# Optimization experiments

Measured on AMD Instinct MI355X. Metric: run time of the kernel, lower is better.

The kernel has to match this reference:

```python
import jax, jax.numpy as jnp
import numpy as np

B, S, H, DK = 2, 2048, 16, 64
D = H * DK  # d_model = 1024


def setup_inputs() -> dict:
    key = jax.random.key(0)
    ks = jax.random.split(key, 12)
    inp = {
        "queries": jax.random.normal(ks[0], (B, S, D), jnp.float32),
        "keys": jax.random.normal(ks[1], (B, S, D), jnp.float32),
        "values": jax.random.normal(ks[2], (B, S, D), jnp.float32),
        # additive 0/1 mask (1 = masked out), causal upper-triangular
        "mask": jnp.triu(jnp.ones((S, S), jnp.float32), k=1)[None, None, :, :],
        "W_q": jax.random.normal(ks[3], (D, D), jnp.float32) / np.sqrt(D),
        "b_q": jnp.zeros((D,), jnp.float32),
        "W_k": jax.random.normal(ks[4], (D, D), jnp.float32) / np.sqrt(D),
        "b_k": jnp.zeros((D,), jnp.float32),
        "W_v": jax.random.normal(ks[5], (D, D), jnp.float32) / np.sqrt(D),
        "b_v": jnp.zeros((D,), jnp.float32),
        "W_o": jax.random.normal(ks[6], (D, D), jnp.float32) / np.sqrt(D),
        "b_o": jnp.zeros((D,), jnp.float32),
    }
    return inp


def _split_heads(x):
    # (B, S, D) -> (B, H, S, DK)
    return x.reshape(x.shape[0], x.shape[1], H, DK).transpose(0, 2, 1, 3)


def reference(queries, keys, values, mask, W_q, b_q, W_k, b_k, W_v, b_v, W_o, b_o):
    q = _split_heads(queries @ W_q + b_q)  # (B, H, S, DK)
    k = _split_heads(keys @ W_k + b_k)
    v = _split_heads(values @ W_v + b_v)
    scale = 1.0 / jnp.sqrt(jnp.asarray(DK, q.dtype))
    scores = jnp.einsum("bhqd,bhkd->bhqk", q, k) * scale  # (B, H, S, S)
    scores = scores + (-1e9) * mask
    weights = jax.nn.softmax(scores, axis=-1)
    o = jnp.einsum("bhqk,bhkd->bhqd", weights, v)  # (B, H, S, DK)
    o = o.transpose(0, 2, 1, 3).reshape(queries.shape[0], queries.shape[1], D)
    return o @ W_o + b_o
```

## Files before the change

### kernel.cpp

```cpp
#include <hip/hip_runtime.h>
#include <hip/hip_bf16.h>
#include <stdint.h>

typedef unsigned short u16;
typedef __attribute__((ext_vector_type(4))) float f32x4;
typedef __attribute__((ext_vector_type(8))) short bf16x8;

#define B_ 2
#define S_ 2048
#define H_ 16
#define D_ 1024
#define XELEMS (B_*S_*D_)
#define WELEMS (D_*D_)
#define QSCALE 0.18033688f

__device__ __forceinline__ u16 f2bf(float f) {
  union { float f; unsigned u; } v; v.f = f;
  unsigned r = v.u + 0x7fffu + ((v.u >> 16) & 1u);
  return (u16)(r >> 16);
}

__device__ __forceinline__ void async16(const void* g, void* l) {
  __builtin_amdgcn_global_load_lds(
      (const __attribute__((address_space(1))) unsigned int*)g,
      (__attribute__((address_space(3))) unsigned int*)l, 16, 0, 0);
}

#if __has_builtin(__builtin_amdgcn_exp2f)
#define EXP2(x) __builtin_amdgcn_exp2f(x)
#else
#define EXP2(x) exp2f(x)
#endif

__device__ __forceinline__ unsigned cvtpk(float a, float b) {
  unsigned r;
  asm("v_cvt_pk_bf16_f32 %0, %1, %2" : "=v"(r) : "v"(a), "v"(b));
  return r;
}

__global__ __launch_bounds__(256) void prep_k(
    const float* __restrict__ q, const float* __restrict__ k,
    const float* __restrict__ v,
    const float* __restrict__ Wq, const float* __restrict__ Wk,
    const float* __restrict__ Wv, const float* __restrict__ Wo,
    u16* __restrict__ X, u16* __restrict__ WT) {
  const int bid = blockIdx.x;
  if (bid < 4096) {
    __shared__ float tile[32][33];
    const int z = bid >> 10, rem = bid & 1023;
    const float* W = (z == 0) ? Wq : (z == 1) ? Wk : (z == 2) ? Wv : Wo;
    u16* o = WT + z * WELEMS;
    const int r0 = (rem >> 5) << 5, c0 = (rem & 31) << 5;
    const int tx = threadIdx.x & 31, ty = threadIdx.x >> 5;
    #pragma unroll
    for (int rr = ty; rr < 32; rr += 8)
      tile[rr][tx] = W[(r0 + rr) * D_ + c0 + tx];
    __syncthreads();
    #pragma unroll
    for (int rr = ty; rr < 32; rr += 8)
      o[(c0 + rr) * D_ + r0 + tx] = f2bf(tile[tx][rr]);
  } else {
    const int cb = bid - 4096;
    const int ngrp = XELEMS / 8;
    const int total = 3 * ngrp;
    for (int i = cb * 256 + threadIdx.x; i < total; i += 1024 * 256) {
      int which = i / ngrp;
      int off = (i - which * ngrp) * 8;
      const float* src = (which == 0) ? q : (which == 1) ? k : v;
      float4 a = *(const float4*)(src + off);
      float4 b = *(const float4*)(src + off + 4);
      u16 rr[8] = {f2bf(a.x), f2bf(a.y), f2bf(a.z), f2bf(a.w),
                   f2bf(b.x), f2bf(b.y), f2bf(b.z), f2bf(b.w)};
      uint4 pk;
      pk.x = (unsigned)rr[0] | ((unsigned)rr[1] << 16);
      pk.y = (unsigned)rr[2] | ((unsigned)rr[3] << 16);
      pk.z = (unsigned)rr[4] | ((unsigned)rr[5] << 16);
      pk.w = (unsigned)rr[6] | ((unsigned)rr[7] << 16);
      *(uint4*)(X + which * XELEMS + off) = pk;
    }
  }
}

template <int MODE, int DBUF>
__device__ __forceinline__ void gemm_body(const u16* __restrict__ A,
                                          const u16* __restrict__ BT,
                                          const float* __restrict__ bias,
                                          void* __restrict__ outp,
                                          int bm, int bn, float scale) {
  constexpr int SMEM_BYTES = DBUF ? 65536 : (MODE == 2 ? 34816 : 32768);
  __shared__ __align__(16) char smem[SMEM_BYTES];
  const int tid = threadIdx.x;
  const int w = tid >> 6, l = tid & 63;
  const int wr = w >> 1, wc = w & 1;
  const int g = l >> 4, r = l & 15;
  (void)w; (void)l;

  f32x4 acc[4][4];
  #pragma unroll
  for (int i = 0; i < 4; i++)
    #pragma unroll
    for (int j = 0; j < 4; j++) acc[i][j] = (f32x4){0.f, 0.f, 0.f, 0.f};

  int dst[4], aoff[4], boff[4];
  #pragma unroll
  for (int i = 0; i < 4; i++) {
    const int o = i * 4096 + tid * 16;
    dst[i] = o;
    const int row = o >> 7;
    const int cbyte = (o & 127) ^ ((row & 7) << 4);
    aoff[i] = (bm + row) * 1024 + (cbyte >> 1);
    boff[i] = (bn + row) * 1024 + (cbyte >> 1);
  }

  if (DBUF == 0) {
    char* Ab = smem;
    char* Bb = smem + 16384;
    for (int t = 0; t < 16; ++t) {
      const int k0 = t * 64;
      #pragma unroll
      for (int i = 0; i < 4; i++) async16(A + aoff[i] + k0, Ab + dst[i]);
      #pragma unroll
      for (int i = 0; i < 4; i++) async16(BT + boff[i] + k0, Bb + dst[i]);
      __syncthreads();
      bf16x8 af[2][4], bf[2][4];
      #pragma unroll
      for (int kk = 0; kk < 2; kk++)
        #pragma unroll
        for (int mi = 0; mi < 4; mi++) {
          const int rA = wr * 64 + mi * 16 + r;
          af[kk][mi] = *(const bf16x8*)(Ab +
              ((rA * 128 + kk * 64 + g * 16) ^ ((rA & 7) << 4)));
        }
      #pragma unroll
      for (int kk = 0; kk < 2; kk++)
        #pragma unroll
        for (int ni = 0; ni < 4; ni++) {
          const int rB = wc * 64 + ni * 16 + r;
          bf[kk][ni] = *(const bf16x8*)(Bb +
              ((rB * 128 + kk * 64 + g * 16) ^ ((rB & 7) << 4)));
        }
      #pragma unroll
      for (int kk = 0; kk < 2; kk++)
        #pragma unroll
        for (int mi = 0; mi < 4; mi++)
          #pragma unroll
          for (int ni = 0; ni < 4; ni++)
            acc[mi][ni] = __builtin_amdgcn_mfma_f32_16x16x32_bf16(
                af[kk][mi], bf[kk][ni], acc[mi][ni], 0, 0, 0);
      __syncthreads();
    }
  } else {
    #pragma unroll
    for (int i = 0; i < 4; i++) {
      async16(A + aoff[i], smem + dst[i]);
      async16(BT + boff[i], smem + 16384 + dst[i]);
    }
    for (int t = 0; t < 16; ++t) {
      const int buf = t & 1;
      const char* Ab = smem + buf * 32768;
      const char* Bb = Ab + 16384;
      if (t < 15) {
        const int k0 = (t + 1) * 64;
        char* An = smem + (buf ^ 1) * 32768;
        #pragma unroll
        for (int i = 0; i < 4; i++) {
          async16(A + aoff[i] + k0, An + dst[i]);
          async16(BT + boff[i] + k0, An + 16384 + dst[i]);
        }
        asm volatile("s_waitcnt vmcnt(8)" ::: "memory");
      } else {
        asm volatile("s_waitcnt vmcnt(0)" ::: "memory");
      }
      asm volatile("s_barrier" ::: "memory");

      bf16x8 af[2][4], bf[2][4];
      #pragma unroll
      for (int kk = 0; kk < 2; kk++)
        #pragma unroll
        for (int mi = 0; mi < 4; mi++) {
          const int rA = wr * 64 + mi * 16 + r;
          af[kk][mi] = *(const bf16x8*)(Ab +
              ((rA * 128 + kk * 64 + g * 16) ^ ((rA & 7) << 4)));
        }
      #pragma unroll
      for (int kk = 0; kk < 2; kk++)
        #pragma unroll
        for (int ni = 0; ni < 4; ni++) {
          const int rB = wc * 64 + ni * 16 + r;
          bf[kk][ni] = *(const bf16x8*)(Bb +
              ((rB * 128 + kk * 64 + g * 16) ^ ((rB & 7) << 4)));
        }
      __builtin_amdgcn_s_setprio(1);
      #pragma unroll
      for (int kk = 0; kk < 2; kk++)
        #pragma unroll
        for (int mi = 0; mi < 4; mi++)
          #pragma unroll
          for (int ni = 0; ni < 4; ni++)
            acc[mi][ni] = __builtin_amdgcn_mfma_f32_16x16x32_bf16(
                af[kk][mi], bf[kk][ni], acc[mi][ni], 0, 0, 0);
      __builtin_amdgcn_s_setprio(0);
      asm volatile("s_barrier" ::: "memory");
    }
  }

  const int col0 = bn + wc * 64;
  float bc[4];
  #pragma unroll
  for (int ni = 0; ni < 4; ni++) bc[ni] = bias[col0 + ni * 16 + r];

  if (MODE == 0) {
    u16* out = (u16*)outp;
    #pragma unroll
    for (int mi = 0; mi < 4; mi++) {
      const int row = bm + wr * 64 + mi * 16 + g * 4;
      #pragma unroll
      for (int ni = 0; ni < 4; ni++) {
        const int col = col0 + ni * 16 + r;
        const int h = col >> 6, dk = col & 63;
        #pragma unroll
        for (int i = 0; i < 4; i++) {
          const int rr = row + i;
          const int b = rr >> 11, s = rr & 2047;
          out[(((b << 4) | h) * 2048 + s) * 64 + dk] =
              f2bf((acc[mi][ni][i] + bc[ni]) * scale);
        }
      }
    }
  } else if (MODE == 2) {
    u16* Ts = (u16*)smem;
    #pragma unroll
    for (int mi = 0; mi < 4; mi++) {
      const int lrow = wr * 64 + mi * 16 + g * 4;
      #pragma unroll
      for (int ni = 0; ni < 4; ni++) {
        const int lcol = wc * 64 + ni * 16 + r;
        u16 p0 = f2bf(acc[mi][ni][0] + bc[ni]);
        u16 p1 = f2bf(acc[mi][ni][1] + bc[ni]);
        u16 p2 = f2bf(acc[mi][ni][2] + bc[ni]);
        u16 p3 = f2bf(acc[mi][ni][3] + bc[ni]);
        uint2 pk;
        pk.x = (unsigned)p0 | ((unsigned)p1 << 16);
        pk.y = (unsigned)p2 | ((unsigned)p3 << 16);
        *(uint2*)&Ts[lcol * 136 + lrow] = pk;
      }
    }
    __syncthreads();
    u16* out = (u16*)outp;
    const int bb = bm >> 11;
    const int sbase = bm & 2047;
    #pragma unroll
    for (int j = 0; j < 8; j++) {
      const int c = (tid >> 6) * 512 + j * 64 + (tid & 63);
      const int dk = c >> 4, sc = c & 15;
      const int col = bn + dk;
      const int h = col >> 6, dkk = col & 63;
      bf16x8 vv = *(const bf16x8*)&Ts[dk * 136 + sc * 8];
      *(bf16x8*)&out[(((size_t)(((bb << 4) | h) * 64 + dkk)) << 11) +
                     sbase + sc * 8] = vv;
    }
  } else {
    float* out = (float*)outp;
    #pragma unroll
    for (int mi = 0; mi < 4; mi++) {
      const int row = bm + wr * 64 + mi * 16 + g * 4;
      #pragma unroll
      for (int ni = 0; ni < 4; ni++) {
        const int col = col0 + ni * 16 + r;
        #pragma unroll
        for (int i = 0; i < 4; i++)
          out[(row + i) * 1024 + col] = acc[mi][ni][i] + bc[ni];
      }
    }
  }
}

__global__ __launch_bounds__(256) void gemm_qkv_k(
    const u16* __restrict__ X, const u16* __restrict__ WT,
    const float* __restrict__ bq, const float* __restrict__ bk,
    const float* __restrict__ bv, u16* __restrict__ QKV) {
  const int z = blockIdx.z;
  const float* bias = (z == 0) ? bq : (z == 1) ? bk : bv;
  if (z == 2)
    gemm_body<2, 0>(X + z * XELEMS, WT + z * WELEMS, bias, QKV + z * XELEMS,
                    blockIdx.x * 128, blockIdx.y * 128, 1.0f);
  else
    gemm_body<0, 0>(X + z * XELEMS, WT + z * WELEMS, bias, QKV + z * XELEMS,
                    blockIdx.x * 128, blockIdx.y * 128,
                    (z == 0) ? QSCALE : 1.0f);
}

__global__ __launch_bounds__(256) void gemm_o_k(
    const u16* __restrict__ O, const u16* __restrict__ WOT,
    const float* __restrict__ bo, float* __restrict__ out) {
  gemm_body<1, 1>(O, WOT, bo, out, blockIdx.x * 128, blockIdx.y * 128, 1.0f);
}

__global__ __launch_bounds__(512) void attn_k(
    const u16* __restrict__ Qh, const u16* __restrict__ Kh,
    const u16* __restrict__ VTh, u16* __restrict__ O) {
  __shared__ __align__(16) char ldsK[2][8192];
  __shared__ __align__(16) char ldsV[2][8192];
  __shared__ __align__(16) u16 ldsP[8][16 * 72];

  const int bh = blockIdx.y;
  const int pj = blockIdx.x;
  const int tid = threadIdx.x;
  const int w = tid >> 6, l = tid & 63;
  const int grp = w >> 2, wg = w & 3;
  const int g = l >> 4, r = l & 15;
  const int b = bh >> 4, h = bh & 15;

  const u16* Qp = Qh + bh * (S_ * 64);
  const char* Kp = (const char*)(Kh + bh * (S_ * 64));
  const char* Vp = (const char*)(VTh + bh * (64 * S_));

  const int o = w * 1024 + l * 16;
  const int kdst = o;
  const int ksrc = o ^ (((o >> 7) & 7) << 4);
  const int vd = o >> 7, vcb = o & 127;
  const int vfix = vd * (S_ * 2) + (vcb ^ ((vd & 7) << 4));
  u16* Pq = &ldsP[w][0];

  const int qt = grp ? (31 - pj) : pj;
  const int q0w = qt * 64 + wg * 16;
  const int my_nt = qt + 1;
  const int nt_max = 32 - pj;
  const int qloc = wg * 16 + r;

  bf16x8 qf[2];
  #pragma unroll
  for (int dh = 0; dh < 2; dh++)
    qf[dh] = *(const bf16x8*)(Qp + (q0w + r) * 64 + dh * 32 + g * 8);
  asm volatile("s_waitcnt vmcnt(0)" ::: "memory");

  f32x4 accT[4];
  #pragma unroll
  for (int dn = 0; dn < 4; dn++) accT[dn] = (f32x4){0.f, 0.f, 0.f, 0.f};
  float mrun = -1e30f, lsum = 0.f;

  async16(Kp + ksrc, &ldsK[0][0] + kdst);
  async16(Vp + vfix, &ldsV[0][0] + kdst);

  for (int t = 0; t < nt_max; ++t) {
    const int buf = t & 1;
    if (t + 1 < nt_max) {
      async16(Kp + (t + 1) * 8192 + ksrc, &ldsK[buf ^ 1][0] + kdst);
      async16(Vp + (t + 1) * 128 + vfix, &ldsV[buf ^ 1][0] + kdst);
      asm volatile("s_waitcnt vmcnt(2)" ::: "memory");
    } else {
      asm volatile("s_waitcnt vmcnt(0)" ::: "memory");
    }
    asm volatile("s_barrier" ::: "memory");

    if (t < my_nt) {
      const char* Kb = &ldsK[buf][0];
      f32x4 sc[4];
      #pragma unroll
      for (int ct = 0; ct < 4; ct++) {
        const int row = ct * 16 + r;
        const int sw = (row & 7) << 4;
        bf16x8 k0 = *(const bf16x8*)(Kb + ((row * 128 + g * 16) ^ sw));
        bf16x8 k1 = *(const bf16x8*)(Kb + ((row * 128 + 64 + g * 16) ^ sw));
        f32x4 z = (f32x4){0.f, 0.f, 0.f, 0.f};
        z = __builtin_amdgcn_mfma_f32_16x16x32_bf16(k0, qf[0], z, 0, 0, 0);
        sc[ct] = __builtin_amdgcn_mfma_f32_16x16x32_bf16(k1, qf[1], z, 0, 0, 0);
      }

      if (t == my_nt - 1) {
        #pragma unroll
        for (int ct = 0; ct < 4; ct++)
          #pragma unroll
          for (int i = 0; i < 4; i++)
            if (ct * 16 + g * 4 + i > qloc) sc[ct][i] = -1e9f;
      }

      float a0 = fmaxf(fmaxf(sc[0][0], sc[0][1]), sc[0][2]);
      float a1 = fmaxf(fmaxf(sc[0][3], sc[1][0]), sc[1][1]);
      float a2 = fmaxf(fmaxf(sc[1][2], sc[1][3]), sc[2][0]);
      float a3 = fmaxf(fmaxf(sc[2][1], sc[2][2]), sc[2][3]);
      float a4 = fmaxf(fmaxf(sc[3][0], sc[3][1]), sc[3][2]);
      float pmax = fmaxf(fmaxf(fmaxf(a0, a1), fmaxf(a2, a3)),
                         fmaxf(a4, sc[3][3]));
      pmax = fmaxf(pmax, __shfl_xor(pmax, 16, 64));
      pmax = fmaxf(pmax, __shfl_xor(pmax, 32, 64));

      if (!__all(pmax - mrun <= 11.0f)) {
        const float mnew = fmaxf(mrun, pmax);
        const float corr = EXP2(mrun - mnew);
        mrun = mnew;
        #pragma unroll
        for (int dn = 0; dn < 4; dn++)
          #pragma unroll
          for (int i = 0; i < 4; i++) accT[dn][i] *= corr;
        lsum *= corr;
      }

      float ps = 0.f;
      #pragma unroll
      for (int ct = 0; ct < 4; ct++)
        #pragma unroll
        for (int i = 0; i < 4; i++) {
          const float p = EXP2(sc[ct][i] - mrun);
          sc[ct][i] = p;
          ps += p;
        }
      ps += __shfl_xor(ps, 16, 64);
      ps += __shfl_xor(ps, 32, 64);
      lsum += ps;

      #pragma unroll
      for (int ct = 0; ct < 4; ct++) {
        uint2 pk;
        pk.x = cvtpk(sc[ct][0], sc[ct][1]);
        pk.y = cvtpk(sc[ct][2], sc[ct][3]);
        *(uint2*)&Pq[r * 72 + ct * 16 + g * 4] = pk;
      }
      asm volatile("s_waitcnt lgkmcnt(0)" ::: "memory");

      const char* Vb = &ldsV[buf][0];
      bf16x8 pf[2];
      #pragma unroll
      for (int kp = 0; kp < 2; kp++)
        pf[kp] = *(const bf16x8*)&Pq[r * 72 + kp * 32 + g * 8];
      __builtin_amdgcn_s_setprio(1);
      #pragma unroll
      for (int dn = 0; dn < 4; dn++) {
        const int vrow = dn * 16 + r;
        const int vsw = (vrow & 7) << 4;
        #pragma unroll
        for (int kp = 0; kp < 2; kp++) {
          bf16x8 vf = *(const bf16x8*)(Vb + ((vrow * 128 + kp * 64 + g * 16) ^ vsw));
          accT[dn] = __builtin_amdgcn_mfma_f32_16x16x32_bf16(vf, pf[kp], accT[dn], 0, 0, 0);
        }
      }
      __builtin_amdgcn_s_setprio(0);
    }
    asm volatile("s_barrier" ::: "memory");
  }

  const float inv = 1.0f / lsum;
  const int qrow = q0w + r;
  #pragma unroll
  for (int dn = 0; dn < 4; dn++) {
    u16 o0 = f2bf(accT[dn][0] * inv), o1 = f2bf(accT[dn][1] * inv);
    u16 o2 = f2bf(accT[dn][2] * inv), o3 = f2bf(accT[dn][3] * inv);
    uint2 pk;
    pk.x = (unsigned)o0 | ((unsigned)o1 << 16);
    pk.y = (unsigned)o2 | ((unsigned)o3 << 16);
    *(uint2*)(O + ((size_t)(b * 2048 + qrow)) * 1024 + h * 64 + dn * 16 + g * 4) = pk;
  }
}

extern "C" void kernel_launch(void* const* d_in, const int* in_sizes, int n_in,
                              void* d_out, int out_size, void* d_ws, size_t ws_size,
                              hipStream_t stream) {
  const float* q  = (const float*)d_in[0];
  const float* k  = (const float*)d_in[1];
  const float* v  = (const float*)d_in[2];
  const float* Wq = (const float*)d_in[4];
  const float* bq = (const float*)d_in[5];
  const float* Wk = (const float*)d_in[6];
  const float* bk = (const float*)d_in[7];
  const float* Wv = (const float*)d_in[8];
  const float* bv = (const float*)d_in[9];
  const float* Wo = (const float*)d_in[10];
  const float* bo = (const float*)d_in[11];

  char* ws = (char*)d_ws;
  const size_t MB = 1u << 20;
  u16* X   = (u16*)(ws);
  u16* WT  = (u16*)(ws + 24 * MB);
  u16* QKV = (u16*)(ws + 32 * MB);
  u16* O   = (u16*)(ws);

  hipLaunchKernelGGL(prep_k, dim3(5120), dim3(256), 0, stream,
                     q, k, v, Wq, Wk, Wv, Wo, X, WT);
  hipLaunchKernelGGL(gemm_qkv_k, dim3(32, 8, 3), dim3(256), 0, stream,
                     X, WT, bq, bk, bv, QKV);
  hipLaunchKernelGGL(attn_k, dim3(16, 32), dim3(512), 0, stream,
                     QKV, QKV + XELEMS, QKV + 2 * XELEMS, O);
  hipLaunchKernelGGL(gemm_o_k, dim3(32, 8), dim3(256), 0, stream,
                     O, WT + 3 * WELEMS, bo, (float*)d_out);
}
```

Before: 124.7 us.

## Triple-buffer attention K/V loads and stage QKV epilogue through LDS

The attention kernel moves from double to triple buffering of K/V tiles, prefetching two tiles ahead so global-to-LDS latency is better hidden behind MFMA work. Separately, the Q/K projection GEMM epilogue now writes bf16 results into an LDS tile and then emits coalesced 16-byte stores into the head-split layout, replacing scattered 2-byte global stores. The cost is more LDS per attention block (48KB K/V plus P), which may reduce occupancy, and an extra barrier plus LDS round trip in the GEMM epilogue.

```diff
diff --git a/kernel.cpp b/kernel.cpp
--- a/kernel.cpp
+++ b/kernel.cpp
@@ -87,7 +87,7 @@
                                           const float* __restrict__ bias,
                                           void* __restrict__ outp,
                                           int bm, int bn, float scale) {
-  constexpr int SMEM_BYTES = DBUF ? 65536 : (MODE == 2 ? 34816 : 32768);
+  constexpr int SMEM_BYTES = DBUF ? 65536 : ((MODE == 0 || MODE == 2) ? 34816 : 32768);
   __shared__ __align__(16) char smem[SMEM_BYTES];
   const int tid = threadIdx.x;
   const int w = tid >> 6, l = tid & 63;
@@ -210,22 +210,31 @@
   for (int ni = 0; ni < 4; ni++) bc[ni] = bias[col0 + ni * 16 + r];
 
   if (MODE == 0) {
+    u16* Ts = (u16*)smem;
+    #pragma unroll
+    for (int mi = 0; mi < 4; mi++) {
+      #pragma unroll
+      for (int ni = 0; ni < 4; ni++) {
+        const int lcol = wc * 64 + ni * 16 + r;
+        #pragma unroll
+        for (int i = 0; i < 4; i++) {
+          const int lrow = wr * 64 + mi * 16 + g * 4 + i;
+          Ts[lrow * 136 + lcol] = f2bf((acc[mi][ni][i] + bc[ni]) * scale);
+        }
+      }
+    }
+    __syncthreads();
     u16* out = (u16*)outp;
-    #pragma unroll
-    for (int mi = 0; mi < 4; mi++) {
-      const int row = bm + wr * 64 + mi * 16 + g * 4;
-      #pragma unroll
-      for (int ni = 0; ni < 4; ni++) {
-        const int col = col0 + ni * 16 + r;
-        const int h = col >> 6, dk = col & 63;
-        #pragma unroll
-        for (int i = 0; i < 4; i++) {
-          const int rr = row + i;
-          const int b = rr >> 11, s = rr & 2047;
-          out[(((b << 4) | h) * 2048 + s) * 64 + dk] =
-              f2bf((acc[mi][ni][i] + bc[ni]) * scale);
-        }
-      }
+    const int bb = bm >> 11;
+    const int sbase = bm & 2047;
+    #pragma unroll
+    for (int j = 0; j < 8; j++) {
+      const int c = j * 256 + tid;
+      const int row = c >> 4, oct = c & 15;
+      const int col = bn + oct * 8;
+      const int h = col >> 6, dk = col & 63;
+      bf16x8 vv = *(const bf16x8*)&Ts[row * 136 + oct * 8];
+      *(bf16x8*)&out[(((size_t)((bb << 4) | h) * 2048 + sbase + row) << 6) + dk] = vv;
     }
   } else if (MODE == 2) {
     u16* Ts = (u16*)smem;
@@ -299,8 +308,8 @@
 __global__ __launch_bounds__(512) void attn_k(
     const u16* __restrict__ Qh, const u16* __restrict__ Kh,
     const u16* __restrict__ VTh, u16* __restrict__ O) {
-  __shared__ __align__(16) char ldsK[2][8192];
-  __shared__ __align__(16) char ldsV[2][8192];
+  __shared__ __align__(16) char ldsK[3][8192];
+  __shared__ __align__(16) char ldsV[3][8192];
   __shared__ __align__(16) u16 ldsP[8][16 * 72];
 
   const int bh = blockIdx.y;
@@ -341,12 +350,16 @@
 
   async16(Kp + ksrc, &ldsK[0][0] + kdst);
   async16(Vp + vfix, &ldsV[0][0] + kdst);
-
+  async16(Kp + 8192 + ksrc, &ldsK[1][0] + kdst);
+  async16(Vp + 128 + vfix, &ldsV[1][0] + kdst);
+
+  int cur = 0, pre = 2;
   for (int t = 0; t < nt_max; ++t) {
-    const int buf = t & 1;
-    if (t + 1 < nt_max) {
-      async16(Kp + (t + 1) * 8192 + ksrc, &ldsK[buf ^ 1][0] + kdst);
-      async16(Vp + (t + 1) * 128 + vfix, &ldsV[buf ^ 1][0] + kdst);
+    if (t + 2 < nt_max) {
+      async16(Kp + (t + 2) * 8192 + ksrc, &ldsK[pre][0] + kdst);
+      async16(Vp + (t + 2) * 128 + vfix, &ldsV[pre][0] + kdst);
+      asm volatile("s_waitcnt vmcnt(4)" ::: "memory");
+    } else if (t + 1 < nt_max) {
       asm volatile("s_waitcnt vmcnt(2)" ::: "memory");
     } else {
       asm volatile("s_waitcnt vmcnt(0)" ::: "memory");
@@ -354,7 +367,7 @@
     asm volatile("s_barrier" ::: "memory");
 
     if (t < my_nt) {
-      const char* Kb = &ldsK[buf][0];
+      const char* Kb = &ldsK[cur][0];
       f32x4 sc[4];
       #pragma unroll
       for (int ct = 0; ct < 4; ct++) {
@@ -418,7 +431,7 @@
       }
       asm volatile("s_waitcnt lgkmcnt(0)" ::: "memory");
 
-      const char* Vb = &ldsV[buf][0];
+      const char* Vb = &ldsV[cur][0];
       bf16x8 pf[2];
       #pragma unroll
       for (int kp = 0; kp < 2; kp++)
@@ -437,6 +450,8 @@
       __builtin_amdgcn_s_setprio(0);
     }
     asm volatile("s_barrier" ::: "memory");
+    cur = (cur == 2) ? 0 : cur + 1;
+    pre = (pre == 2) ? 0 : pre + 1;
   }
 
   const float inv = 1.0f / lsum;
```

Measured after the change: 128.2 us. 2.8% more time.
